# Kernel optimization log

Measured on AMD Instinct MI355X. Metric: run time of the kernel, lower is better.

The kernel has to match this reference:

```python
import jax, jax.numpy as jnp
import numpy as np

B, IN = 16, 8192          # batch, network input size
C, A, N = 64, 512, 512    # cores, axons/core, neurons/core
OUT = 1024                # output sources
T = 32                    # simulation_length


def setup_inputs() -> dict:
    key = jax.random.key(0)
    ks = jax.random.split(key, 7)
    x = jax.random.uniform(ks[0], (B, IN), jnp.float32)
    W = jax.random.normal(ks[1], (C, N, A), jnp.float32) * 0.05  # core_matrix.T per core
    thresholds = jnp.ones((C,), jnp.float32)
    # axon routing: src_core == -1 -> read from input spikes, else from core buffer
    src_core = jax.random.randint(ks[2], (C, A), -1, C, dtype=jnp.int32)
    src_idx_in = jax.random.randint(ks[3], (C, A), 0, IN, dtype=jnp.int32)
    src_idx_buf = jax.random.randint(ks[4], (C, A), 0, N, dtype=jnp.int32)
    src_index = jnp.where(src_core < 0, src_idx_in, src_idx_buf)
    out_src_core = jax.random.randint(ks[5], (OUT,), 0, C, dtype=jnp.int32)
    out_src_index = jax.random.randint(ks[6], (OUT,), 0, N, dtype=jnp.int32)
    return dict(x=x, W=W, thresholds=thresholds, src_core=src_core,
                src_index=src_index, out_src_core=out_src_core,
                out_src_index=out_src_index)


def _uniform_spikes(x, cycle, T_):
    # faithful port of to_uniform_spikes
    Nspk = jnp.round(x * T_).astype(jnp.int32)
    Ti = jnp.int32(T_)
    mask = (Nspk != 0) & (Nspk != Ti) & (cycle < T_)
    Nsafe = jnp.maximum(Nspk, 1)
    spacing = T_ / Nsafe.astype(x.dtype)
    res = mask & (jnp.floor(cycle / spacing) < Nsafe.astype(x.dtype)) & (jnp.floor(jnp.mod(cycle, spacing)) == 0)
    return jnp.where(Nspk == Ti, jnp.ones((), x.dtype), res.astype(x.dtype))


def reference(x, W, thresholds, src_core, src_index, out_src_core, out_src_index):
    Bc = x.shape[0]
    is_input = src_core < 0                       # (C, A)
    buf_flat_idx = (jnp.maximum(src_core, 0) * N + src_index).reshape(-1)  # (C*A,)
    in_idx = src_index.reshape(-1)                # (C*A,)
    out_flat_idx = out_src_core * N + out_src_index  # (OUT,)
    th = thresholds[:, None, None]                # (C, 1, 1)

    def step(carry, cycle):
        memb, buffers = carry                     # each (C, B, N)
        spikes = _uniform_spikes(x, cycle.astype(x.dtype), jnp.float32(T))  # (B, IN)
        # gather axon signals (irregular access across all cores' buffers + input)
        buf_flat = jnp.swapaxes(buffers, 0, 1).reshape(Bc, C * N)
        from_buf = buf_flat[:, buf_flat_idx].reshape(Bc, C, A)
        from_in = spikes[:, in_idx].reshape(Bc, C, A)
        signals = jnp.where(is_input[None, :, :], from_in, from_buf)  # (B, C, A)
        # memb += core_matrix.T @ signals  (per core)
        memb = memb + jnp.einsum('cna,bca->cbn', W, signals)
        fired = th < memb                         # thresholding_mode '<'
        buffers = fired.astype(x.dtype)
        memb = jnp.where(fired, memb - th, memb)  # firing_mode 'Default'
        # scatter fired buffers into output counts
        buf_flat2 = jnp.swapaxes(buffers, 0, 1).reshape(Bc, C * N)
        out_inc = buf_flat2[:, out_flat_idx]      # (B, OUT)
        return (memb, buffers), out_inc

    memb0 = jnp.zeros((C, Bc, N), x.dtype)
    buf0 = jnp.zeros((C, Bc, N), x.dtype)
    (_, _), outs = jax.lax.scan(step, (memb0, buf0), jnp.arange(T))
    return outs.sum(axis=0)  # spike counts (B, OUT)
```

## Files before the change

kernel.cpp:

```cpp
#include <hip/hip_runtime.h>
#include <stdint.h>

#define Bb   16
#define INn  8192
#define Cc   64
#define Aa   512
#define Nn   512
#define OUTo 1024
#define Tt   32

__global__ void spike_kernel(const float* __restrict__ x,
                             uint32_t* __restrict__ spk) {
    int idx = blockIdx.x * 256 + threadIdx.x;
    if (idx >= Bb * INn) return;
    float xv = x[idx];
    float nf = rintf(xv * 32.0f);
    int nspk = (int)nf;
    uint32_t m;
    if (nspk >= 32) {
        m = 0xFFFFFFFFu;
    } else if (nspk <= 0) {
        m = 0u;
    } else {
        float spacing = 32.0f / nf;
        m = 0u;
        #pragma unroll
        for (int t = 0; t < 32; ++t) {
            float ct = (float)t;
            bool fire = (floorf(ct / spacing) < nf) &&
                        (floorf(fmodf(ct, spacing)) == 0.0f);
            if (fire) m |= (1u << t);
        }
    }
    spk[idx] = m;
}

__global__ __launch_bounds__(256) void cycle_kernel(
        const float* __restrict__ W,
        const float* __restrict__ thr,
        const int* __restrict__ src_core,
        const int* __restrict__ src_index,
        const uint32_t* __restrict__ spk,
        uint32_t* __restrict__ buf,
        float* __restrict__ memb,
        int t) {
    const int c   = blockIdx.x;
    const int tid = threadIdx.x;
    const int nl  = tid & 127;
    const int bh  = tid >> 7;
    const int n   = blockIdx.y * 128 + nl;

    __shared__ float sig[Aa * Bb];

    const int base = c * Aa;
    for (int idx = tid; idx < Aa * Bb; idx += 256) {
        int a = idx >> 4;
        int b = idx & 15;
        int sc = src_core[base + a];
        int si = src_index[base + a];
        uint32_t bit;
        if (sc < 0) {
            bit = (spk[b * INn + si] >> t) & 1u;
        } else {
            bit = (t > 0) ? ((buf[(sc * Bb + b) * Nn + si] >> (t - 1)) & 1u)
                          : 0u;
        }
        sig[a * Bb + b] = (float)bit;
    }
    __syncthreads();

    float acc[8];
    #pragma unroll
    for (int j = 0; j < 8; ++j) acc[j] = 0.0f;

    const float* wrow = W + (size_t)(c * Nn + n) * Aa;
    const int sb = bh * 8;

    for (int a0 = 0; a0 < Aa; a0 += 4) {
        float4 w4 = *(const float4*)(wrow + a0);
        float4 s00 = *(const float4*)(&sig[(a0 + 0) * Bb + sb]);
        float4 s01 = *(const float4*)(&sig[(a0 + 0) * Bb + sb + 4]);
        float4 s10 = *(const float4*)(&sig[(a0 + 1) * Bb + sb]);
        float4 s11 = *(const float4*)(&sig[(a0 + 1) * Bb + sb + 4]);
        float4 s20 = *(const float4*)(&sig[(a0 + 2) * Bb + sb]);
        float4 s21 = *(const float4*)(&sig[(a0 + 2) * Bb + sb + 4]);
        float4 s30 = *(const float4*)(&sig[(a0 + 3) * Bb + sb]);
        float4 s31 = *(const float4*)(&sig[(a0 + 3) * Bb + sb + 4]);
        acc[0] += w4.x * s00.x; acc[1] += w4.x * s00.y;
        acc[2] += w4.x * s00.z; acc[3] += w4.x * s00.w;
        acc[4] += w4.x * s01.x; acc[5] += w4.x * s01.y;
        acc[6] += w4.x * s01.z; acc[7] += w4.x * s01.w;
        acc[0] += w4.y * s10.x; acc[1] += w4.y * s10.y;
        acc[2] += w4.y * s10.z; acc[3] += w4.y * s10.w;
        acc[4] += w4.y * s11.x; acc[5] += w4.y * s11.y;
        acc[6] += w4.y * s11.z; acc[7] += w4.y * s11.w;
        acc[0] += w4.z * s20.x; acc[1] += w4.z * s20.y;
        acc[2] += w4.z * s20.z; acc[3] += w4.z * s20.w;
        acc[4] += w4.z * s21.x; acc[5] += w4.z * s21.y;
        acc[6] += w4.z * s21.z; acc[7] += w4.z * s21.w;
        acc[0] += w4.w * s30.x; acc[1] += w4.w * s30.y;
        acc[2] += w4.w * s30.z; acc[3] += w4.w * s30.w;
        acc[4] += w4.w * s31.x; acc[5] += w4.w * s31.y;
        acc[6] += w4.w * s31.z; acc[7] += w4.w * s31.w;
    }

    const float th = thr[c];
    #pragma unroll
    for (int j = 0; j < 8; ++j) {
        int b = sb + j;
        size_t off = (size_t)(c * Bb + b) * Nn + n;
        float m = memb[off] + acc[j];
        uint32_t wd = buf[off];
        if (th < m) {
            m -= th;
            wd |= (1u << t);
        }
        memb[off] = m;
        buf[off] = wd;
    }
}

__global__ void out_kernel(const uint32_t* __restrict__ buf,
                           const int* __restrict__ oc,
                           const int* __restrict__ oi,
                           float* __restrict__ out) {
    int idx = blockIdx.x * 256 + threadIdx.x;
    if (idx >= Bb * OUTo) return;
    int b = idx / OUTo;
    int o = idx - b * OUTo;
    uint32_t wd = buf[(oc[o] * Bb + b) * Nn + oi[o]];
    out[idx] = (float)__popc(wd);
}

extern "C" void kernel_launch(void* const* d_in, const int* in_sizes, int n_in,
                              void* d_out, int out_size, void* d_ws,
                              size_t ws_size, hipStream_t stream) {
    const float* x         = (const float*)d_in[0];
    const float* W         = (const float*)d_in[1];
    const float* thr       = (const float*)d_in[2];
    const int*   src_core  = (const int*)d_in[3];
    const int*   src_index = (const int*)d_in[4];
    const int*   osc       = (const int*)d_in[5];
    const int*   osi       = (const int*)d_in[6];
    float* out = (float*)d_out;

    uint32_t* spk  = (uint32_t*)d_ws;
    uint32_t* buf  = (uint32_t*)((char*)d_ws + (size_t)Bb * INn * 4);
    float*    memb = (float*)((char*)d_ws + (size_t)Bb * INn * 4
                                          + (size_t)Cc * Bb * Nn * 4);

    hipMemsetAsync(buf, 0, (size_t)Cc * Bb * Nn * 4 * 2, stream);

    spike_kernel<<<dim3((Bb * INn) / 256), 256, 0, stream>>>(x, spk);

    for (int t = 0; t < Tt; ++t) {
        cycle_kernel<<<dim3(Cc, 4), 256, 0, stream>>>(
            W, thr, src_core, src_index, spk, buf, memb, t);
    }

    out_kernel<<<dim3((Bb * OUTo + 255) / 256), 256, 0, stream>>>(
        buf, osc, osi, out);
}
```

Measured before the change: 1.206 ms.

## Split axon gather into separate kernel and read signals via scalar loads

Moves the per-core axon signal gather out of the cycle kernel into its own grid-wide kernel that writes a global signal array. The cycle kernel then reads signals through wave-uniform addresses (readfirstlane on the batch half) so they can become scalar loads, and runs with smaller blocks over twice as many tiles. The goal is to spread the gather across the whole GPU instead of serialising it per block before the matmul, and to raise occupancy. The cost is an extra kernel launch per cycle plus a global round trip for the signal array.

```diff
diff --git a/kernel.cpp b/kernel.cpp
--- a/kernel.cpp
+++ b/kernel.cpp
@@ -35,79 +35,65 @@
     spk[idx] = m;
 }
 
-__global__ __launch_bounds__(256) void cycle_kernel(
+__global__ void gather_kernel(const int* __restrict__ src_core,
+                              const int* __restrict__ src_index,
+                              const uint32_t* __restrict__ spk,
+                              const uint32_t* __restrict__ buf,
+                              float* __restrict__ sig, int t) {
+    int idx = blockIdx.x * 256 + threadIdx.x;
+    int b  = idx & 15;
+    int ca = idx >> 4;
+    int sc = src_core[ca];
+    int si = src_index[ca];
+    float v;
+    if (sc < 0) {
+        v = (float)((spk[b * INn + si] >> t) & 1u);
+    } else {
+        v = (t > 0) ? (float)((buf[(sc * Bb + b) * Nn + si] >> (t - 1)) & 1u)
+                    : 0.0f;
+    }
+    sig[ca * 16 + b] = v;
+}
+
+__global__ __launch_bounds__(128) void cycle_kernel(
         const float* __restrict__ W,
         const float* __restrict__ thr,
-        const int* __restrict__ src_core,
-        const int* __restrict__ src_index,
-        const uint32_t* __restrict__ spk,
+        const float* __restrict__ sig,
         uint32_t* __restrict__ buf,
         float* __restrict__ memb,
         int t) {
-    const int c   = blockIdx.x;
-    const int tid = threadIdx.x;
-    const int nl  = tid & 127;
-    const int bh  = tid >> 7;
-    const int n   = blockIdx.y * 128 + nl;
+    const int c  = blockIdx.x;
+    const int bh = __builtin_amdgcn_readfirstlane(threadIdx.x >> 6);
+    const int n  = blockIdx.y * 64 + (threadIdx.x & 63);
 
-    __shared__ float sig[Aa * Bb];
-
-    const int base = c * Aa;
-    for (int idx = tid; idx < Aa * Bb; idx += 256) {
-        int a = idx >> 4;
-        int b = idx & 15;
-        int sc = src_core[base + a];
-        int si = src_index[base + a];
-        uint32_t bit;
-        if (sc < 0) {
-            bit = (spk[b * INn + si] >> t) & 1u;
-        } else {
-            bit = (t > 0) ? ((buf[(sc * Bb + b) * Nn + si] >> (t - 1)) & 1u)
-                          : 0u;
-        }
-        sig[a * Bb + b] = (float)bit;
-    }
-    __syncthreads();
+    const float* __restrict__ wrow = W + (size_t)(c * Nn + n) * Aa;
+    const float* __restrict__ sgc  = sig + c * Aa * 16 + bh * 8;
 
     float acc[8];
     #pragma unroll
     for (int j = 0; j < 8; ++j) acc[j] = 0.0f;
 
-    const float* wrow = W + (size_t)(c * Nn + n) * Aa;
-    const int sb = bh * 8;
-
     for (int a0 = 0; a0 < Aa; a0 += 4) {
         float4 w4 = *(const float4*)(wrow + a0);
-        float4 s00 = *(const float4*)(&sig[(a0 + 0) * Bb + sb]);
-        float4 s01 = *(const float4*)(&sig[(a0 + 0) * Bb + sb + 4]);
-        float4 s10 = *(const float4*)(&sig[(a0 + 1) * Bb + sb]);
-        float4 s11 = *(const float4*)(&sig[(a0 + 1) * Bb + sb + 4]);
-        float4 s20 = *(const float4*)(&sig[(a0 + 2) * Bb + sb]);
-        float4 s21 = *(const float4*)(&sig[(a0 + 2) * Bb + sb + 4]);
-        float4 s30 = *(const float4*)(&sig[(a0 + 3) * Bb + sb]);
-        float4 s31 = *(const float4*)(&sig[(a0 + 3) * Bb + sb + 4]);
-        acc[0] += w4.x * s00.x; acc[1] += w4.x * s00.y;
-        acc[2] += w4.x * s00.z; acc[3] += w4.x * s00.w;
-        acc[4] += w4.x * s01.x; acc[5] += w4.x * s01.y;
-        acc[6] += w4.x * s01.z; acc[7] += w4.x * s01.w;
-        acc[0] += w4.y * s10.x; acc[1] += w4.y * s10.y;
-        acc[2] += w4.y * s10.z; acc[3] += w4.y * s10.w;
-        acc[4] += w4.y * s11.x; acc[5] += w4.y * s11.y;
-        acc[6] += w4.y * s11.z; acc[7] += w4.y * s11.w;
-        acc[0] += w4.z * s20.x; acc[1] += w4.z * s20.y;
-        acc[2] += w4.z * s20.z; acc[3] += w4.z * s20.w;
-        acc[4] += w4.z * s21.x; acc[5] += w4.z * s21.y;
-        acc[6] += w4.z * s21.z; acc[7] += w4.z * s21.w;
-        acc[0] += w4.w * s30.x; acc[1] += w4.w * s30.y;
-        acc[2] += w4.w * s30.z; acc[3] += w4.w * s30.w;
-        acc[4] += w4.w * s31.x; acc[5] += w4.w * s31.y;
-        acc[6] += w4.w * s31.z; acc[7] += w4.w * s31.w;
+        #pragma unroll
+        for (int k = 0; k < 4; ++k) {
+            float w = (k == 0) ? w4.x : (k == 1) ? w4.y : (k == 2) ? w4.z : w4.w;
+            const float* sa = sgc + (size_t)(a0 + k) * 16;
+            acc[0] += w * sa[0];
+            acc[1] += w * sa[1];
+            acc[2] += w * sa[2];
+            acc[3] += w * sa[3];
+            acc[4] += w * sa[4];
+            acc[5] += w * sa[5];
+            acc[6] += w * sa[6];
+            acc[7] += w * sa[7];
+        }
     }
 
     const float th = thr[c];
     #pragma unroll
     for (int j = 0; j < 8; ++j) {
-        int b = sb + j;
+        int b = bh * 8 + j;
         size_t off = (size_t)(c * Bb + b) * Nn + n;
         float m = memb[off] + acc[j];
         uint32_t wd = buf[off];
@@ -144,18 +130,21 @@
     const int*   osi       = (const int*)d_in[6];
     float* out = (float*)d_out;
 
-    uint32_t* spk  = (uint32_t*)d_ws;
-    uint32_t* buf  = (uint32_t*)((char*)d_ws + (size_t)Bb * INn * 4);
-    float*    memb = (float*)((char*)d_ws + (size_t)Bb * INn * 4
-                                          + (size_t)Cc * Bb * Nn * 4);
+    char* p = (char*)d_ws;
+    uint32_t* spk  = (uint32_t*)p;                 p += (size_t)Bb * INn * 4;
+    uint32_t* buf  = (uint32_t*)p;                 p += (size_t)Cc * Bb * Nn * 4;
+    float*    memb = (float*)p;                    p += (size_t)Cc * Bb * Nn * 4;
+    float*    sig  = (float*)p;
 
     hipMemsetAsync(buf, 0, (size_t)Cc * Bb * Nn * 4 * 2, stream);
 
     spike_kernel<<<dim3((Bb * INn) / 256), 256, 0, stream>>>(x, spk);
 
     for (int t = 0; t < Tt; ++t) {
-        cycle_kernel<<<dim3(Cc, 4), 256, 0, stream>>>(
-            W, thr, src_core, src_index, spk, buf, memb, t);
+        gather_kernel<<<dim3((Cc * Aa * Bb) / 256), 256, 0, stream>>>(
+            src_core, src_index, spk, buf, sig, t);
+        cycle_kernel<<<dim3(Cc, 8), 128, 0, stream>>>(
+            W, thr, sig, buf, memb, t);
     }
 
     out_kernel<<<dim3((Bb * OUTo + 255) / 256), 256, 0, stream>>>(
```

New measurement: 1.344 ms. +11.5%, slower.
